# Kernel tuning notes

Hardware: AMD Instinct MI355X
Metric: run time of the kernel (lower is better)

Reference implementation:

```python
import jax, jax.numpy as jnp
import numpy as np

NEG_SLOPE = 0.2
LN_EPS = 1e-5


def _gat_layer(x, src, dst, W, a_src, a_dst, N):
    # x: [N, Fin], W: [Fin, H*C], a_src/a_dst: [H, C]
    H, C = a_src.shape
    h = (x @ W).reshape(N, H, C)
    al_src = (h * a_src).sum(-1)  # [N, H]
    al_dst = (h * a_dst).sum(-1)  # [N, H]
    e = jax.nn.leaky_relu(al_src[src] + al_dst[dst], NEG_SLOPE)  # [E, H]
    m = jax.ops.segment_max(e, dst, num_segments=N)
    e = jnp.exp(e - m[dst])
    denom = jax.ops.segment_sum(e, dst, num_segments=N)
    alpha = e / denom[dst]  # softmax over incoming edges per dst node
    msg = h[src] * alpha[:, :, None]  # [E, H, C]
    return jax.ops.segment_sum(msg, dst, num_segments=N)  # [N, H, C]


def _layer_norm(x, g, b):
    mu = x.mean(-1, keepdims=True)
    var = ((x - mu) ** 2).mean(-1, keepdims=True)
    return (x - mu) * jax.lax.rsqrt(var + LN_EPS) * g + b


def setup_inputs() -> dict:
    key = jax.random.key(0)
    ks = jax.random.split(key, 20)
    N, E, Fin, Ch, H = 50000, 800000, 128, 64, 4
    s = lambda k, shp, sc=0.05: jax.random.normal(k, shp, dtype=jnp.float32) * sc
    return {
        "x": jax.random.normal(ks[0], (N, Fin), dtype=jnp.float32),
        "edge_index": jax.random.randint(ks[1], (2, E), 0, N, dtype=jnp.int64),
        "W1": s(ks[2], (Fin, H * Ch)),
        "att_src1": s(ks[3], (H, Ch)),
        "att_dst1": s(ks[4], (H, Ch)),
        "b1": jnp.zeros((H * Ch,), jnp.float32),
        "ln1_g": jnp.ones((H * Ch,), jnp.float32),
        "ln1_b": jnp.zeros((H * Ch,), jnp.float32),
        "W2": s(ks[5], (H * Ch, Ch)),
        "att_src2": s(ks[6], (1, Ch)),
        "att_dst2": s(ks[7], (1, Ch)),
        "b2": jnp.zeros((Ch,), jnp.float32),
        "ln2_g": jnp.ones((Ch,), jnp.float32),
        "ln2_b": jnp.zeros((Ch,), jnp.float32),
        "fc1_W": s(ks[8], (Ch, Ch // 2)),
        "fc1_b": jnp.zeros((Ch // 2,), jnp.float32),
        "fc2_W": s(ks[9], (Ch // 2, 1)),
        "fc2_b": jnp.zeros((1,), jnp.float32),
    }


def reference(x, edge_index, W1, att_src1, att_dst1, b1, ln1_g, ln1_b,
              W2, att_src2, att_dst2, b2, ln2_g, ln2_b,
              fc1_W, fc1_b, fc2_W, fc2_b):
    N = x.shape[0]
    # PyG GATConv adds self-loops by default
    loop = jnp.arange(N, dtype=edge_index.dtype)
    src = jnp.concatenate([edge_index[0], loop])
    dst = jnp.concatenate([edge_index[1], loop])

    # GAT layer 1 (heads=4, concat) + LayerNorm + ReLU (dropout is identity in eval)
    h = _gat_layer(x, src, dst, W1, att_src1, att_dst1, N).reshape(N, -1) + b1
    h = jax.nn.relu(_layer_norm(h, ln1_g, ln1_b))

    # GAT layer 2 (heads=1) + LayerNorm + ReLU
    h = _gat_layer(h, src, dst, W2, att_src2, att_dst2, N).reshape(N, -1) + b2
    h = jax.nn.relu(_layer_norm(h, ln2_g, ln2_b))

    # MLP head
    h = jax.nn.relu(h @ fc1_W + fc1_b)
    return h @ fc2_W + fc2_b  # [N, 1]
```

## Files before the change

### kernel.cpp

```cpp
#include <hip/hip_runtime.h>
#include <hip/hip_fp16.h>
#include <math.h>

#define NEG_SLOPE 0.2f
#define LN_EPS 1e-5f
#define SCCHUNK 1024
#define PADCAP 64

typedef __attribute__((ext_vector_type(8))) _Float16 half8;
typedef __attribute__((ext_vector_type(4))) _Float16 half4;
typedef __attribute__((ext_vector_type(4))) float floatx4;

static __device__ __forceinline__ float lrelu(float e) {
    return e > 0.0f ? e : NEG_SLOPE * e;
}

__global__ __launch_bounds__(256) void k_g1sc(
    const float* __restrict__ x, const float* __restrict__ W1,
    const float* __restrict__ as1, const float* __restrict__ ad1,
    _Float16* __restrict__ h1, float* __restrict__ als, float* __restrict__ ald,
    const int* __restrict__ ei, unsigned* __restrict__ cursor, int* __restrict__ eidx,
    int N, int E, int nsc)
{
    const int tid = threadIdx.x;

    if ((int)blockIdx.x < nsc) {
        const int Et = E + N;
        const int i0 = blockIdx.x * SCCHUNK;
#pragma unroll
        for (int j = 0; j < SCCHUNK / 256; ++j) {
            int i = i0 + j * 256 + tid;
            if (i < Et) {
                int s, d;
                if (i < E) { s = ei[i]; d = ei[E + i]; } else { s = d = i - E; }
                unsigned pos = atomicAdd(&cursor[d], 1u);
                if (pos < PADCAP) eidx[(size_t)d * PADCAP + pos] = s;
            }
        }
        return;
    }

    const int tile = blockIdx.x - nsc;
    const int lane = tid & 63, w = tid >> 6;
    const int l15 = lane & 15, quad = lane >> 4;
    const int r_base = tile * 64;

    half8 B[4][4];
    float asv[4], adv[4];
#pragma unroll
    for (int nt = 0; nt < 4; ++nt) {
        const int n = w * 64 + nt * 16 + l15;
        asv[nt] = as1[n]; adv[nt] = ad1[n];
#pragma unroll
        for (int ks = 0; ks < 4; ++ks) {
            const int k0 = ks * 32 + quad * 8;
            half8 b;
#pragma unroll
            for (int j = 0; j < 8; ++j) b[j] = (_Float16)W1[(size_t)(k0 + j) * 256 + n];
            B[ks][nt] = b;
        }
    }

#pragma unroll
    for (int rt = 0; rt < 4; ++rt) {
        const int r0 = r_base + rt * 16;
        int m = r0 + l15; if (m >= N) m = N - 1;
        half8 A[4];
#pragma unroll
        for (int ks = 0; ks < 4; ++ks) {
            const int k0 = ks * 32 + quad * 8;
            const float4* xp = (const float4*)(x + (size_t)m * 128 + k0);
            float4 v0 = xp[0], v1 = xp[1];
            half8 a;
            a[0] = (_Float16)v0.x; a[1] = (_Float16)v0.y; a[2] = (_Float16)v0.z; a[3] = (_Float16)v0.w;
            a[4] = (_Float16)v1.x; a[5] = (_Float16)v1.y; a[6] = (_Float16)v1.z; a[7] = (_Float16)v1.w;
            A[ks] = a;
        }
        floatx4 C[4];
#pragma unroll
        for (int nt = 0; nt < 4; ++nt) C[nt] = (floatx4){0.f, 0.f, 0.f, 0.f};
#pragma unroll
        for (int ks = 0; ks < 4; ++ks)
#pragma unroll
            for (int nt = 0; nt < 4; ++nt)
                C[nt] = __builtin_amdgcn_mfma_f32_16x16x32_f16(A[ks], B[ks][nt], C[nt], 0, 0, 0);

#pragma unroll
        for (int reg = 0; reg < 4; ++reg) {
            const int row = r0 + quad * 4 + reg;
            float vs = 0.f, vd = 0.f;
#pragma unroll
            for (int nt = 0; nt < 4; ++nt) {
                float c = C[nt][reg];
                if (row < N) h1[(size_t)row * 256 + w * 64 + nt * 16 + l15] = (_Float16)c;
                vs += c * asv[nt]; vd += c * adv[nt];
            }
#pragma unroll
            for (int o = 1; o < 16; o <<= 1) { vs += __shfl_xor(vs, o); vd += __shfl_xor(vd, o); }
            if (l15 == 0 && row < N) { als[row * 4 + w] = vs; ald[row * 4 + w] = vd; }
        }
    }
}

__global__ __launch_bounds__(256) void k_agg1(
    const _Float16* __restrict__ h1, const float* __restrict__ als, const float* __restrict__ ald,
    const unsigned* __restrict__ cursor, const int* __restrict__ eidx,
    const float* __restrict__ b1, const float* __restrict__ g1, const float* __restrict__ be1,
    _Float16* __restrict__ hln1, int N)
{
    const int wv = threadIdx.x >> 6, lane = threadIdx.x & 63;
    int n = blockIdx.x * 4 + wv;
    if (n >= N) n = N - 1;
    const int base = n * PADCAP;
    int deg = (int)cursor[n]; if (deg > PADCAP) deg = PADCAP;
    const float4 ad = ((const float4*)ald)[n];

    float m0 = -1e30f, m1 = -1e30f, m2 = -1e30f, m3 = -1e30f;
    float s0 = 0.f, s1 = 0.f, s2 = 0.f, s3 = 0.f;
    if (lane < deg) {
        int src = eidx[base + lane];
        float4 a4 = ((const float4*)als)[src];
        m0 = lrelu(a4.x + ad.x); s0 = 1.f;
        m1 = lrelu(a4.y + ad.y); s1 = 1.f;
        m2 = lrelu(a4.z + ad.z); s2 = 1.f;
        m3 = lrelu(a4.w + ad.w); s3 = 1.f;
    }
#pragma unroll
    for (int o = 32; o; o >>= 1) {
        float mo, so, nm;
        mo = __shfl_xor(m0, o); so = __shfl_xor(s0, o);
        nm = fmaxf(m0, mo); s0 = s0 * __expf(m0 - nm) + so * __expf(mo - nm); m0 = nm;
        mo = __shfl_xor(m1, o); so = __shfl_xor(s1, o);
        nm = fmaxf(m1, mo); s1 = s1 * __expf(m1 - nm) + so * __expf(mo - nm); m1 = nm;
        mo = __shfl_xor(m2, o); so = __shfl_xor(s2, o);
        nm = fmaxf(m2, mo); s2 = s2 * __expf(m2 - nm) + so * __expf(mo - nm); m2 = nm;
        mo = __shfl_xor(m3, o); so = __shfl_xor(s3, o);
        nm = fmaxf(m3, mo); s3 = s3 * __expf(m3 - nm) + so * __expf(mo - nm); m3 = nm;
    }

    const int hd = lane >> 4, l15 = lane & 15;
    const float mh  = hd == 0 ? m0 : (hd == 1 ? m1 : (hd == 2 ? m2 : m3));
    const float sh_ = hd == 0 ? s0 : (hd == 1 ? s1 : (hd == 2 ? s2 : s3));
    const float adh = hd == 0 ? ad.x : (hd == 1 ? ad.y : (hd == 2 ? ad.z : ad.w));
    const float cc = -mh - __logf(sh_);

    float4 acc = make_float4(0.f, 0.f, 0.f, 0.f);
    const int bp_base = (lane & 48) << 2;
    for (int c0 = 0; c0 < deg; c0 += 16) {
        int nc = deg - c0; if (nc > 16) nc = 16;
        int j = c0 + l15; if (j >= deg) j = deg - 1;
        int srcv = eidx[base + j];
        float alpha = __expf(lrelu(als[srcv * 4 + hd] + adh) + cc);
        if (l15 >= nc) alpha = 0.f;
        for (int e0 = 0; e0 < nc; e0 += 4) {
#pragma unroll
            for (int u = 0; u < 4; ++u) {
                const int e = e0 + u;
                int s = __builtin_amdgcn_readlane(srcv, e);
                float a_e = __int_as_float(
                    __builtin_amdgcn_ds_bpermute(bp_base + e * 4, __float_as_int(alpha)));
                half4 v = *(const half4*)(h1 + (size_t)s * 256 + 4 * lane);
                acc.x = fmaf((float)v.x, a_e, acc.x);
                acc.y = fmaf((float)v.y, a_e, acc.y);
                acc.z = fmaf((float)v.z, a_e, acc.z);
                acc.w = fmaf((float)v.w, a_e, acc.w);
            }
        }
    }

    float4 bb = ((const float4*)b1)[lane];
    float y0 = acc.x + bb.x, y1 = acc.y + bb.y, y2 = acc.z + bb.z, y3 = acc.w + bb.w;
    float ps = y0 + y1 + y2 + y3;
    float pss = y0 * y0 + y1 * y1 + y2 * y2 + y3 * y3;
#pragma unroll
    for (int o = 32; o; o >>= 1) { ps += __shfl_xor(ps, o); pss += __shfl_xor(pss, o); }
    float mu = ps * (1.f / 256.f);
    float var = pss * (1.f / 256.f) - mu * mu;
    float rstd = rsqrtf(var + LN_EPS);
    float4 gg = ((const float4*)g1)[lane];
    float4 b2v = ((const float4*)be1)[lane];
    half4 outv;
    outv.x = (_Float16)fmaxf((y0 - mu) * rstd * gg.x + b2v.x, 0.f);
    outv.y = (_Float16)fmaxf((y1 - mu) * rstd * gg.y + b2v.y, 0.f);
    outv.z = (_Float16)fmaxf((y2 - mu) * rstd * gg.z + b2v.z, 0.f);
    outv.w = (_Float16)fmaxf((y3 - mu) * rstd * gg.w + b2v.w, 0.f);
    ((half4*)(hln1 + (size_t)n * 256))[lane] = outv;
}

__global__ __launch_bounds__(256) void k_gemm2(
    const _Float16* __restrict__ hln1, const float* __restrict__ W2,
    const float* __restrict__ as2, const float* __restrict__ ad2,
    _Float16* __restrict__ h2, float* __restrict__ als2, float* __restrict__ ald2, int N)
{
    __shared__ float ps_s[4][64], ps_d[4][64];
    const int lane = threadIdx.x & 63, w = threadIdx.x >> 6;
    const int l15 = lane & 15, quad = lane >> 4;
    const int r_base = blockIdx.x * 64;

    const int n = w * 16 + l15;
    const float asv = as2[n], adv = ad2[n];
    half8 B[8];
#pragma unroll
    for (int ks = 0; ks < 8; ++ks) {
        const int k0 = ks * 32 + quad * 8;
        half8 b;
#pragma unroll
        for (int j = 0; j < 8; ++j) b[j] = (_Float16)W2[(size_t)(k0 + j) * 64 + n];
        B[ks] = b;
    }

#pragma unroll
    for (int rt = 0; rt < 4; ++rt) {
        const int r0 = r_base + rt * 16;
        int m = r0 + l15; if (m >= N) m = N - 1;
        floatx4 C = (floatx4){0.f, 0.f, 0.f, 0.f};
#pragma unroll
        for (int ks = 0; ks < 8; ++ks) {
            half8 a = *(const half8*)(hln1 + (size_t)m * 256 + ks * 32 + quad * 8);
            C = __builtin_amdgcn_mfma_f32_16x16x32_f16(a, B[ks], C, 0, 0, 0);
        }
#pragma unroll
        for (int reg = 0; reg < 4; ++reg) {
            const int row = r0 + quad * 4 + reg;
            float c = C[reg];
            if (row < N) h2[(size_t)row * 64 + n] = (_Float16)c;
            float vs = c * asv, vd = c * adv;
#pragma unroll
            for (int o = 1; o < 16; o <<= 1) { vs += __shfl_xor(vs, o); vd += __shfl_xor(vd, o); }
            if (l15 == 0) {
                ps_s[w][rt * 16 + quad * 4 + reg] = vs;
                ps_d[w][rt * 16 + quad * 4 + reg] = vd;
            }
        }
    }
    __syncthreads();
    const int t = threadIdx.x;
    if (t < 64) {
        const int row = r_base + t;
        if (row < N) {
            als2[row] = ps_s[0][t] + ps_s[1][t] + ps_s[2][t] + ps_s[3][t];
            ald2[row] = ps_d[0][t] + ps_d[1][t] + ps_d[2][t] + ps_d[3][t];
        }
    }
}

__global__ __launch_bounds__(256) void k_agg2(
    const _Float16* __restrict__ h2, const float* __restrict__ als, const float* __restrict__ ald,
    const unsigned* __restrict__ cursor, const int* __restrict__ eidx,
    const float* __restrict__ b2, const float* __restrict__ g2, const float* __restrict__ be2,
    const float* __restrict__ fc1W, const float* __restrict__ fc1b,
    const float* __restrict__ fc2W, const float* __restrict__ fc2b,
    float* __restrict__ out, int N)
{
    __shared__ float sh[4][64];
    const int wv = threadIdx.x >> 6, lane = threadIdx.x & 63;
    int n = blockIdx.x * 4 + wv;
    if (n >= N) n = N - 1;
    const int base = n * PADCAP;
    int deg = (int)cursor[n]; if (deg > PADCAP) deg = PADCAP;
    const float adn = ald[n];

    float m = -1e30f, s = 0.f;
    int srcv = eidx[base + (lane < deg ? lane : deg - 1)];
    if (lane < deg) { m = lrelu(als[srcv] + adn); s = 1.f; }
#pragma unroll
    for (int o = 32; o; o >>= 1) {
        float mo = __shfl_xor(m, o), so = __shfl_xor(s, o);
        float nm = fmaxf(m, mo);
        s = s * __expf(m - nm) + so * __expf(mo - nm); m = nm;
    }
    const float cc = -m - __logf(s);

    float alpha = __expf(lrelu(als[srcv] + adn) + cc);
    if (lane >= deg) alpha = 0.f;
    float acc = 0.f;
    for (int e0 = 0; e0 < deg; e0 += 4) {
#pragma unroll
        for (int u = 0; u < 4; ++u) {
            const int e = e0 + u;
            int sidx = __builtin_amdgcn_readlane(srcv, e);
            float a_e = __int_as_float(
                __builtin_amdgcn_readlane(__float_as_int(alpha), e));
            acc = fmaf((float)h2[(size_t)sidx * 64 + lane], a_e, acc);
        }
    }

    float y = acc + b2[lane];
    float ps = y, pss = y * y;
#pragma unroll
    for (int o = 32; o; o >>= 1) { ps += __shfl_xor(ps, o); pss += __shfl_xor(pss, o); }
    float mu = ps * (1.f / 64.f);
    float var = pss * (1.f / 64.f) - mu * mu;
    float r = fmaxf((y - mu) * rsqrtf(var + LN_EPS) * g2[lane] + be2[lane], 0.f);

    sh[wv][lane] = r;

    if (lane < 32) {
        float a1 = fc1b[lane];
#pragma unroll 8
        for (int k = 0; k < 64; ++k) a1 += sh[wv][k] * fc1W[k * 32 + lane];
        a1 = fmaxf(a1, 0.f);
        float t = a1 * fc2W[lane];
#pragma unroll
        for (int o = 16; o; o >>= 1) t += __shfl_xor(t, o);
        if (lane == 0) out[n] = t + fc2b[0];
    }
}

extern "C" void kernel_launch(void* const* d_in, const int* in_sizes, int n_in,
                              void* d_out, int out_size, void* d_ws, size_t ws_size,
                              hipStream_t stream)
{
    const float* x   = (const float*)d_in[0];
    const int* ei    = (const int*)d_in[1];
    const float* W1  = (const float*)d_in[2];
    const float* as1 = (const float*)d_in[3];
    const float* ad1 = (const float*)d_in[4];
    const float* b1  = (const float*)d_in[5];
    const float* g1  = (const float*)d_in[6];
    const float* be1 = (const float*)d_in[7];
    const float* W2  = (const float*)d_in[8];
    const float* as2 = (const float*)d_in[9];
    const float* ad2 = (const float*)d_in[10];
    const float* b2  = (const float*)d_in[11];
    const float* g2  = (const float*)d_in[12];
    const float* be2 = (const float*)d_in[13];
    const float* fc1W = (const float*)d_in[14];
    const float* fc1b = (const float*)d_in[15];
    const float* fc2W = (const float*)d_in[16];
    const float* fc2b = (const float*)d_in[17];
    float* out = (float*)d_out;

    const int N = in_sizes[0] / 128;
    const int E = in_sizes[1] / 2;
    const int Et = E + N;
    const int nsc = (Et + SCCHUNK - 1) / SCCHUNK;
    const int ntiles = (N + 63) / 64;

    char* p = (char*)d_ws;
    auto carve = [&](size_t bytes) {
        void* q = p;
        p += (bytes + 255) & ~(size_t)255;
        return q;
    };
    _Float16* h1    = (_Float16*)carve((size_t)N * 256 * 2);
    _Float16* hln1h = (_Float16*)carve((size_t)N * 256 * 2);
    _Float16* h2    = (_Float16*)carve((size_t)N * 64 * 2);
    float* als1 = (float*)carve((size_t)N * 4 * 4);
    float* ald1 = (float*)carve((size_t)N * 4 * 4);
    float* als2 = (float*)carve((size_t)N * 4);
    float* ald2 = (float*)carve((size_t)N * 4);
    unsigned* cursor = (unsigned*)carve((size_t)N * 4);
    int* eidx   = (int*)carve((size_t)N * PADCAP * 4);

    hipMemsetAsync(cursor, 0, (size_t)N * 4, stream);
    k_g1sc<<<nsc + ntiles, 256, 0, stream>>>(x, W1, as1, ad1, h1, als1, ald1,
                                             ei, cursor, eidx, N, E, nsc);
    k_agg1<<<(N + 3) / 4, 256, 0, stream>>>(h1, als1, ald1, cursor, eidx, b1, g1, be1, hln1h, N);
    k_gemm2<<<(N + 63) / 64, 256, 0, stream>>>(hln1h, W2, as2, ad2, h2, als2, ald2, N);
    k_agg2<<<(N + 3) / 4, 256, 0, stream>>>(h2, als2, ald2, cursor, eidx,
                                            b2, g2, be2, fc1W, fc1b, fc2W, fc2b, out, N);
}
```

Before: 324.5 us.

## Fuse layer-1 aggregation with layer-2 GEMM via LDS tile; enlarge scatter chunks

Merges the layer-1 attention aggregation and LayerNorm kernel with the layer-2 projection GEMM. Each block aggregates 16 nodes into a padded LDS tile, then runs the MFMA directly from LDS, so the N×256 fp16 intermediate is never written to or reread from global memory and one launch is dropped. The trade-off is that the W2 fragments are now loaded once per 16 rows instead of once per 64, and there are 4× fewer waves per node batch. The edge-scatter chunk also grows from 1024 to 8192 edges per block, cutting the number of scatter blocks.

Result: faster. 301.4 us (-7.1%).

```diff
diff --git a/kernel.cpp b/kernel.cpp
--- a/kernel.cpp
+++ b/kernel.cpp
@@ -4,8 +4,9 @@
 
 #define NEG_SLOPE 0.2f
 #define LN_EPS 1e-5f
-#define SCCHUNK 1024
+#define SCCHUNK 8192
 #define PADCAP 64
+#define HSTR 264
 
 typedef __attribute__((ext_vector_type(8))) _Float16 half8;
 typedef __attribute__((ext_vector_type(4))) _Float16 half4;
@@ -27,7 +28,7 @@
     if ((int)blockIdx.x < nsc) {
         const int Et = E + N;
         const int i0 = blockIdx.x * SCCHUNK;
-#pragma unroll
+#pragma unroll 4
         for (int j = 0; j < SCCHUNK / 256; ++j) {
             int i = i0 + j * 256 + tid;
             if (i < Et) {
@@ -102,144 +103,137 @@
     }
 }
 
-__global__ __launch_bounds__(256) void k_agg1(
+__global__ __launch_bounds__(256) void k_agg1g2(
     const _Float16* __restrict__ h1, const float* __restrict__ als, const float* __restrict__ ald,
     const unsigned* __restrict__ cursor, const int* __restrict__ eidx,
     const float* __restrict__ b1, const float* __restrict__ g1, const float* __restrict__ be1,
-    _Float16* __restrict__ hln1, int N)
-{
-    const int wv = threadIdx.x >> 6, lane = threadIdx.x & 63;
-    int n = blockIdx.x * 4 + wv;
-    if (n >= N) n = N - 1;
-    const int base = n * PADCAP;
-    int deg = (int)cursor[n]; if (deg > PADCAP) deg = PADCAP;
-    const float4 ad = ((const float4*)ald)[n];
-
-    float m0 = -1e30f, m1 = -1e30f, m2 = -1e30f, m3 = -1e30f;
-    float s0 = 0.f, s1 = 0.f, s2 = 0.f, s3 = 0.f;
-    if (lane < deg) {
-        int src = eidx[base + lane];
-        float4 a4 = ((const float4*)als)[src];
-        m0 = lrelu(a4.x + ad.x); s0 = 1.f;
-        m1 = lrelu(a4.y + ad.y); s1 = 1.f;
-        m2 = lrelu(a4.z + ad.z); s2 = 1.f;
-        m3 = lrelu(a4.w + ad.w); s3 = 1.f;
-    }
-#pragma unroll
-    for (int o = 32; o; o >>= 1) {
-        float mo, so, nm;
-        mo = __shfl_xor(m0, o); so = __shfl_xor(s0, o);
-        nm = fmaxf(m0, mo); s0 = s0 * __expf(m0 - nm) + so * __expf(mo - nm); m0 = nm;
-        mo = __shfl_xor(m1, o); so = __shfl_xor(s1, o);
-        nm = fmaxf(m1, mo); s1 = s1 * __expf(m1 - nm) + so * __expf(mo - nm); m1 = nm;
-        mo = __shfl_xor(m2, o); so = __shfl_xor(s2, o);
-        nm = fmaxf(m2, mo); s2 = s2 * __expf(m2 - nm) + so * __expf(mo - nm); m2 = nm;
-        mo = __shfl_xor(m3, o); so = __shfl_xor(s3, o);
-        nm = fmaxf(m3, mo); s3 = s3 * __expf(m3 - nm) + so * __expf(mo - nm); m3 = nm;
-    }
-
-    const int hd = lane >> 4, l15 = lane & 15;
-    const float mh  = hd == 0 ? m0 : (hd == 1 ? m1 : (hd == 2 ? m2 : m3));
-    const float sh_ = hd == 0 ? s0 : (hd == 1 ? s1 : (hd == 2 ? s2 : s3));
-    const float adh = hd == 0 ? ad.x : (hd == 1 ? ad.y : (hd == 2 ? ad.z : ad.w));
-    const float cc = -mh - __logf(sh_);
-
-    float4 acc = make_float4(0.f, 0.f, 0.f, 0.f);
-    const int bp_base = (lane & 48) << 2;
-    for (int c0 = 0; c0 < deg; c0 += 16) {
-        int nc = deg - c0; if (nc > 16) nc = 16;
-        int j = c0 + l15; if (j >= deg) j = deg - 1;
-        int srcv = eidx[base + j];
-        float alpha = __expf(lrelu(als[srcv * 4 + hd] + adh) + cc);
-        if (l15 >= nc) alpha = 0.f;
-        for (int e0 = 0; e0 < nc; e0 += 4) {
-#pragma unroll
-            for (int u = 0; u < 4; ++u) {
-                const int e = e0 + u;
-                int s = __builtin_amdgcn_readlane(srcv, e);
-                float a_e = __int_as_float(
-                    __builtin_amdgcn_ds_bpermute(bp_base + e * 4, __float_as_int(alpha)));
-                half4 v = *(const half4*)(h1 + (size_t)s * 256 + 4 * lane);
-                acc.x = fmaf((float)v.x, a_e, acc.x);
-                acc.y = fmaf((float)v.y, a_e, acc.y);
-                acc.z = fmaf((float)v.z, a_e, acc.z);
-                acc.w = fmaf((float)v.w, a_e, acc.w);
-            }
-        }
-    }
-
-    float4 bb = ((const float4*)b1)[lane];
-    float y0 = acc.x + bb.x, y1 = acc.y + bb.y, y2 = acc.z + bb.z, y3 = acc.w + bb.w;
-    float ps = y0 + y1 + y2 + y3;
-    float pss = y0 * y0 + y1 * y1 + y2 * y2 + y3 * y3;
-#pragma unroll
-    for (int o = 32; o; o >>= 1) { ps += __shfl_xor(ps, o); pss += __shfl_xor(pss, o); }
-    float mu = ps * (1.f / 256.f);
-    float var = pss * (1.f / 256.f) - mu * mu;
-    float rstd = rsqrtf(var + LN_EPS);
-    float4 gg = ((const float4*)g1)[lane];
-    float4 b2v = ((const float4*)be1)[lane];
-    half4 outv;
-    outv.x = (_Float16)fmaxf((y0 - mu) * rstd * gg.x + b2v.x, 0.f);
-    outv.y = (_Float16)fmaxf((y1 - mu) * rstd * gg.y + b2v.y, 0.f);
-    outv.z = (_Float16)fmaxf((y2 - mu) * rstd * gg.z + b2v.z, 0.f);
-    outv.w = (_Float16)fmaxf((y3 - mu) * rstd * gg.w + b2v.w, 0.f);
-    ((half4*)(hln1 + (size_t)n * 256))[lane] = outv;
-}
-
-__global__ __launch_bounds__(256) void k_gemm2(
-    const _Float16* __restrict__ hln1, const float* __restrict__ W2,
-    const float* __restrict__ as2, const float* __restrict__ ad2,
+    const float* __restrict__ W2, const float* __restrict__ as2, const float* __restrict__ ad2,
     _Float16* __restrict__ h2, float* __restrict__ als2, float* __restrict__ ald2, int N)
 {
-    __shared__ float ps_s[4][64], ps_d[4][64];
-    const int lane = threadIdx.x & 63, w = threadIdx.x >> 6;
-    const int l15 = lane & 15, quad = lane >> 4;
-    const int r_base = blockIdx.x * 64;
-
-    const int n = w * 16 + l15;
-    const float asv = as2[n], adv = ad2[n];
-    half8 B[8];
-#pragma unroll
-    for (int ks = 0; ks < 8; ++ks) {
-        const int k0 = ks * 32 + quad * 8;
-        half8 b;
-#pragma unroll
-        for (int j = 0; j < 8; ++j) b[j] = (_Float16)W2[(size_t)(k0 + j) * 64 + n];
-        B[ks] = b;
-    }
-
-#pragma unroll
-    for (int rt = 0; rt < 4; ++rt) {
-        const int r0 = r_base + rt * 16;
-        int m = r0 + l15; if (m >= N) m = N - 1;
+    __shared__ _Float16 hlds[16 * HSTR];
+    __shared__ float ps_s[4][16], ps_d[4][16];
+    const int wv = threadIdx.x >> 6, lane = threadIdx.x & 63;
+    const int base = blockIdx.x * 16;
+    const int hd = lane >> 4, l15 = lane & 15;
+
+    for (int it = 0; it < 4; ++it) {
+        int n = base + wv * 4 + it;
+        if (n >= N) n = N - 1;
+        const int ebase = n * PADCAP;
+        int deg = (int)cursor[n]; if (deg > PADCAP) deg = PADCAP;
+        const float4 ad = ((const float4*)ald)[n];
+
+        float m0 = -1e30f, m1 = -1e30f, m2 = -1e30f, m3 = -1e30f;
+        float s0 = 0.f, s1 = 0.f, s2 = 0.f, s3 = 0.f;
+        if (lane < deg) {
+            int src = eidx[ebase + lane];
+            float4 a4 = ((const float4*)als)[src];
+            m0 = lrelu(a4.x + ad.x); s0 = 1.f;
+            m1 = lrelu(a4.y + ad.y); s1 = 1.f;
+            m2 = lrelu(a4.z + ad.z); s2 = 1.f;
+            m3 = lrelu(a4.w + ad.w); s3 = 1.f;
+        }
+#pragma unroll
+        for (int o = 32; o; o >>= 1) {
+            float mo, so, nm;
+            mo = __shfl_xor(m0, o); so = __shfl_xor(s0, o);
+            nm = fmaxf(m0, mo); s0 = s0 * __expf(m0 - nm) + so * __expf(mo - nm); m0 = nm;
+            mo = __shfl_xor(m1, o); so = __shfl_xor(s1, o);
+            nm = fmaxf(m1, mo); s1 = s1 * __expf(m1 - nm) + so * __expf(mo - nm); m1 = nm;
+            mo = __shfl_xor(m2, o); so = __shfl_xor(s2, o);
+            nm = fmaxf(m2, mo); s2 = s2 * __expf(m2 - nm) + so * __expf(mo - nm); m2 = nm;
+            mo = __shfl_xor(m3, o); so = __shfl_xor(s3, o);
+            nm = fmaxf(m3, mo); s3 = s3 * __expf(m3 - nm) + so * __expf(mo - nm); m3 = nm;
+        }
+
+        const float mh  = hd == 0 ? m0 : (hd == 1 ? m1 : (hd == 2 ? m2 : m3));
+        const float sh_ = hd == 0 ? s0 : (hd == 1 ? s1 : (hd == 2 ? s2 : s3));
+        const float adh = hd == 0 ? ad.x : (hd == 1 ? ad.y : (hd == 2 ? ad.z : ad.w));
+        const float cc = -mh - __logf(sh_);
+
+        float4 acc = make_float4(0.f, 0.f, 0.f, 0.f);
+        const int bp_base = (lane & 48) << 2;
+        for (int c0 = 0; c0 < deg; c0 += 16) {
+            int nc = deg - c0; if (nc > 16) nc = 16;
+            int j = c0 + l15; if (j >= deg) j = deg - 1;
+            int srcv = eidx[ebase + j];
+            float alpha = __expf(lrelu(als[srcv * 4 + hd] + adh) + cc);
+            if (l15 >= nc) alpha = 0.f;
+            for (int e0 = 0; e0 < nc; e0 += 4) {
+#pragma unroll
+                for (int u = 0; u < 4; ++u) {
+                    const int e = e0 + u;
+                    int s = __builtin_amdgcn_readlane(srcv, e);
+                    float a_e = __int_as_float(
+                        __builtin_amdgcn_ds_bpermute(bp_base + e * 4, __float_as_int(alpha)));
+                    half4 v = *(const half4*)(h1 + (size_t)s * 256 + 4 * lane);
+                    acc.x = fmaf((float)v.x, a_e, acc.x);
+                    acc.y = fmaf((float)v.y, a_e, acc.y);
+                    acc.z = fmaf((float)v.z, a_e, acc.z);
+                    acc.w = fmaf((float)v.w, a_e, acc.w);
+                }
+            }
+        }
+
+        float4 bb = ((const float4*)b1)[lane];
+        float y0 = acc.x + bb.x, y1 = acc.y + bb.y, y2 = acc.z + bb.z, y3 = acc.w + bb.w;
+        float ps = y0 + y1 + y2 + y3;
+        float pss = y0 * y0 + y1 * y1 + y2 * y2 + y3 * y3;
+#pragma unroll
+        for (int o = 32; o; o >>= 1) { ps += __shfl_xor(ps, o); pss += __shfl_xor(pss, o); }
+        float mu = ps * (1.f / 256.f);
+        float var = pss * (1.f / 256.f) - mu * mu;
+        float rstd = rsqrtf(var + LN_EPS);
+        float4 gg = ((const float4*)g1)[lane];
+        float4 b2v = ((const float4*)be1)[lane];
+        half4 outv;
+        outv.x = (_Float16)fmaxf((y0 - mu) * rstd * gg.x + b2v.x, 0.f);
+        outv.y = (_Float16)fmaxf((y1 - mu) * rstd * gg.y + b2v.y, 0.f);
+        outv.z = (_Float16)fmaxf((y2 - mu) * rstd * gg.z + b2v.z, 0.f);
+        outv.w = (_Float16)fmaxf((y3 - mu) * rstd * gg.w + b2v.w, 0.f);
+        ((half4*)(hlds + (wv * 4 + it) * HSTR))[lane] = outv;
+    }
+    __syncthreads();
+
+    const int quad = lane >> 4;
+    {
+        const int n = wv * 16 + l15;
+        const float asv = as2[n], adv = ad2[n];
+        half8 B[8];
+#pragma unroll
+        for (int ks = 0; ks < 8; ++ks) {
+            const int k0 = ks * 32 + quad * 8;
+            half8 b;
+#pragma unroll
+            for (int j = 0; j < 8; ++j) b[j] = (_Float16)W2[(size_t)(k0 + j) * 64 + n];
+            B[ks] = b;
+        }
         floatx4 C = (floatx4){0.f, 0.f, 0.f, 0.f};
 #pragma unroll
         for (int ks = 0; ks < 8; ++ks) {
-            half8 a = *(const half8*)(hln1 + (size_t)m * 256 + ks * 32 + quad * 8);
+            half8 a = *(const half8*)(hlds + l15 * HSTR + ks * 32 + quad * 8);
             C = __builtin_amdgcn_mfma_f32_16x16x32_f16(a, B[ks], C, 0, 0, 0);
         }
 #pragma unroll
         for (int reg = 0; reg < 4; ++reg) {
-            const int row = r0 + quad * 4 + reg;
+            const int rowl = quad * 4 + reg;
+            const int grow = base + rowl;
             float c = C[reg];
-            if (row < N) h2[(size_t)row * 64 + n] = (_Float16)c;
+            if (grow < N) h2[(size_t)grow * 64 + n] = (_Float16)c;
             float vs = c * asv, vd = c * adv;
 #pragma unroll
             for (int o = 1; o < 16; o <<= 1) { vs += __shfl_xor(vs, o); vd += __shfl_xor(vd, o); }
-            if (l15 == 0) {
-                ps_s[w][rt * 16 + quad * 4 + reg] = vs;
-                ps_d[w][rt * 16 + quad * 4 + reg] = vd;
-            }
+            if (l15 == 0) { ps_s[wv][rowl] = vs; ps_d[wv][rowl] = vd; }
         }
     }
     __syncthreads();
-    const int t = threadIdx.x;
-    if (t < 64) {
-        const int row = r_base + t;
-        if (row < N) {
-            als2[row] = ps_s[0][t] + ps_s[1][t] + ps_s[2][t] + ps_s[3][t];
-            ald2[row] = ps_d[0][t] + ps_d[1][t] + ps_d[2][t] + ps_d[3][t];
+    if (threadIdx.x < 16) {
+        const int grow = base + threadIdx.x;
+        if (grow < N) {
+            als2[grow] = ps_s[0][threadIdx.x] + ps_s[1][threadIdx.x]
+                       + ps_s[2][threadIdx.x] + ps_s[3][threadIdx.x];
+            ald2[grow] = ps_d[0][threadIdx.x] + ps_d[1][threadIdx.x]
+                       + ps_d[2][threadIdx.x] + ps_d[3][threadIdx.x];
         }
     }
 }
@@ -343,9 +337,8 @@
         p += (bytes + 255) & ~(size_t)255;
         return q;
     };
-    _Float16* h1    = (_Float16*)carve((size_t)N * 256 * 2);
-    _Float16* hln1h = (_Float16*)carve((size_t)N * 256 * 2);
-    _Float16* h2    = (_Float16*)carve((size_t)N * 64 * 2);
+    _Float16* h1 = (_Float16*)carve((size_t)N * 256 * 2);
+    _Float16* h2 = (_Float16*)carve((size_t)N * 64 * 2);
     float* als1 = (float*)carve((size_t)N * 4 * 4);
     float* ald1 = (float*)carve((size_t)N * 4 * 4);
     float* als2 = (float*)carve((size_t)N * 4);
@@ -356,8 +349,9 @@
     hipMemsetAsync(cursor, 0, (size_t)N * 4, stream);
     k_g1sc<<<nsc + ntiles, 256, 0, stream>>>(x, W1, as1, ad1, h1, als1, ald1,
                                              ei, cursor, eidx, N, E, nsc);
-    k_agg1<<<(N + 3) / 4, 256, 0, stream>>>(h1, als1, ald1, cursor, eidx, b1, g1, be1, hln1h, N);
-    k_gemm2<<<(N + 63) / 64, 256, 0, stream>>>(hln1h, W2, as2, ad2, h2, als2, ald2, N);
+    k_agg1g2<<<(N + 15) / 16, 256, 0, stream>>>(h1, als1, ald1, cursor, eidx,
+                                                b1, g1, be1, W2, as2, ad2,
+                                                h2, als2, ald2, N);
     k_agg2<<<(N + 3) / 4, 256, 0, stream>>>(h2, als2, ald2, cursor, eidx,
                                             b2, g2, be2, fc1W, fc1b, fc2W, fc2b, out, N);
 }
```
